# Performance work log

Hardware: AMD Instinct MI355X
Metric: run time of the kernel (lower is better)

Reference implementation:

```python
import jax, jax.numpy as jnp
import numpy as np

NUM_HEADS = 16
WINDOW = 256


def setup_inputs() -> dict:
    key = jax.random.key(0)
    ks = jax.random.split(key, 9)
    B, S, H = 2, 2048, 1024
    sc = 0.02
    return {
        "hidden_states": jax.random.normal(ks[0], (B, S, H), jnp.float32),
        "wq": jax.random.normal(ks[1], (H, H), jnp.float32) * sc,
        "bq": jax.random.normal(ks[2], (H,), jnp.float32) * sc,
        "wk": jax.random.normal(ks[3], (H, H), jnp.float32) * sc,
        "bk": jax.random.normal(ks[4], (H,), jnp.float32) * sc,
        "wv": jax.random.normal(ks[5], (H, H), jnp.float32) * sc,
        "bv": jax.random.normal(ks[6], (H,), jnp.float32) * sc,
        "wo": jax.random.normal(ks[7], (H, H), jnp.float32) * sc,
        "bo": jax.random.normal(ks[8], (H,), jnp.float32) * sc,
    }


def reference(hidden_states, wq, bq, wk, bk, wv, bv, wo, bo):
    B, S, H = hidden_states.shape
    nH, hd = NUM_HEADS, H // NUM_HEADS
    scale = 1.0 / np.sqrt(hd).astype(np.float32)

    def heads(x):  # [B,S,H] -> [B,nH,S,hd]
        return x.reshape(B, S, nH, hd).transpose(0, 2, 1, 3)

    q = heads(hidden_states @ wq.T + bq)
    k = heads(hidden_states @ wk.T + bk)
    v = heads(hidden_states @ wv.T + bv)

    scores = jnp.einsum("bhqd,bhkd->bhqk", q, k) * scale  # [B,nH,S,S]

    # allowed keys for query i: j in [i - WINDOW, i] (causal window)
    i = jnp.arange(S)[:, None]
    j = jnp.arange(S)[None, :]
    allowed = (j <= i) & (j >= i - WINDOW)  # [S,S]

    scores = jnp.where(allowed[None, None], scores, -jnp.inf)
    # original clamps AFTER masking -> -inf becomes -10000 (soft mask)
    scores = jnp.clip(scores, -10000.0, 10000.0)

    probs = jax.nn.softmax(scores, axis=-1)
    probs = jnp.nan_to_num(probs, nan=0.0, posinf=0.0, neginf=0.0)

    out = jnp.einsum("bhqk,bhkd->bhqd", probs, v)  # [B,nH,S,hd]
    out = out.transpose(0, 2, 1, 3).reshape(B, S, H)
    return out @ wo.T + bo
```

## Files before the change

kernel.cpp:

```cpp
#include <hip/hip_runtime.h>
#include <hip/hip_bf16.h>
#include <stdint.h>

typedef __attribute__((ext_vector_type(8))) short short8;
typedef __attribute__((ext_vector_type(4))) float f32x4;
typedef __attribute__((ext_vector_type(4))) unsigned short u16x4;

__device__ __forceinline__ float bf2f(unsigned short u) {
  union { unsigned int u; float f; } x; x.u = ((unsigned int)u) << 16; return x.f;
}
__device__ __forceinline__ unsigned short f2bf(float f) {
  union { float f; unsigned int u; } x; x.f = f;
  unsigned int u = x.u;
  return (unsigned short)((u + 0x7fffu + ((u >> 16) & 1u)) >> 16);
}

__device__ __forceinline__ void gload_lds16(const void* g, void* l) {
  __builtin_amdgcn_global_load_lds(
      (const __attribute__((address_space(1))) void*)g,
      (__attribute__((address_space(3))) void*)l, 16, 0, 0);
}

__global__ void cvt_all(const float* __restrict__ X,
                        const float* __restrict__ w0, const float* __restrict__ w1,
                        const float* __restrict__ w2, const float* __restrict__ w3,
                        unsigned short* __restrict__ Xb,
                        unsigned short* __restrict__ Wb) {
  if (blockIdx.y == 0) {
    int i = (blockIdx.x * 256 + threadIdx.x) * 4;
    f32x4 f = *(const f32x4*)(X + i);
    u16x4 o = { f2bf(f[0]), f2bf(f[1]), f2bf(f[2]), f2bf(f[3]) };
    *(u16x4*)(Xb + i) = o;
  } else {
    int wi = blockIdx.x >> 10;
    const float* s = wi == 0 ? w0 : wi == 1 ? w1 : wi == 2 ? w2 : w3;
    int j = ((blockIdx.x & 1023) * 256 + threadIdx.x) * 4;
    f32x4 f = *(const f32x4*)(s + j);
    u16x4 o = { f2bf(f[0]), f2bf(f[1]), f2bf(f[2]), f2bf(f[3]) };
    *(u16x4*)(Wb + ((size_t)wi << 20) + j) = o;
  }
}

template <int MODE, bool SWAP, int BN>
__device__ __forceinline__ void gemm_body(
    const unsigned short* __restrict__ A, const unsigned short* __restrict__ W,
    const float* __restrict__ bias, unsigned short* __restrict__ obf,
    float* __restrict__ of32, unsigned short* lds, int z) {
  const int K = 1024, NT = 32;
  constexpr int GX = 1024 / BN;
  constexpr int LB = BN / 64;
  constexpr int NWC = BN / 64;
  constexpr int NWR = 4 / NWC;
  constexpr int MS = 128 / NWR;
  constexpr int MR = MS / 16;
  constexpr int ASZ = 128 * 32, BSZ = BN * 32;

  constexpr int NWG = GX * 32;
  int flat = blockIdx.y * GX + blockIdx.x;
  int swz = (flat & 7) * (NWG / 8) + (flat >> 3);
  const int n0 = (swz % GX) * BN, m0 = (swz / GX) * 128;

  const int tid = threadIdx.x, lane = tid & 63, w = tid >> 6;
  const int wr = w / NWC, wc = w % NWC;
  const int fr = lane & 15, g = lane >> 4;

  f32x4 acc[MR][4] = {};

#define STAGE(bi, t)                                                            \
  do {                                                                          \
    unsigned short* lb = lds + (bi) * (ASZ + BSZ);                              \
    _Pragma("unroll") for (int i = 0; i < 2; ++i) {                             \
      int s = i * 256 + tid;                                                    \
      int row = s >> 2;                                                         \
      int gc = (s & 3) ^ ((row >> 1) & 3);                                      \
      gload_lds16(A + (size_t)(m0 + row) * K + (t) * 32 + gc * 8, &lb[s * 8]);  \
    }                                                                           \
    _Pragma("unroll") for (int i = 0; i < LB; ++i) {                            \
      int s = i * 256 + tid;                                                    \
      int row = s >> 2;                                                         \
      int gc = (s & 3) ^ ((row >> 1) & 3);                                      \
      gload_lds16(W + (size_t)(n0 + row) * K + (t) * 32 + gc * 8,               \
                  &lb[ASZ + s * 8]);                                            \
    }                                                                           \
  } while (0)

#define COMPUTE(bi)                                                             \
  do {                                                                          \
    unsigned short* lb = lds + (bi) * (ASZ + BSZ);                              \
    short8 af[MR], bfr[4];                                                      \
    _Pragma("unroll") for (int m = 0; m < MR; ++m) {                            \
      int ra = wr * MS + m * 16 + fr;                                           \
      af[m] = *(const short8*)&lb[ra * 32 + ((g ^ ((ra >> 1) & 3)) * 8)];       \
    }                                                                           \
    _Pragma("unroll") for (int n = 0; n < 4; ++n) {                             \
      int rb2 = wc * 64 + n * 16 + fr;                                          \
      bfr[n] = *(const short8*)&lb[ASZ + rb2 * 32 + ((g ^ ((rb2 >> 1) & 3)) * 8)]; \
    }                                                                           \
    _Pragma("unroll") for (int m = 0; m < MR; ++m)                              \
        _Pragma("unroll") for (int n = 0; n < 4; ++n) {                         \
      if constexpr (SWAP)                                                       \
        acc[m][n] = __builtin_amdgcn_mfma_f32_16x16x32_bf16(bfr[n], af[m],      \
                                                            acc[m][n], 0, 0, 0);\
      else                                                                      \
        acc[m][n] = __builtin_amdgcn_mfma_f32_16x16x32_bf16(af[m], bfr[n],      \
                                                            acc[m][n], 0, 0, 0);\
    }                                                                           \
  } while (0)

  STAGE(0, 0);
  STAGE(1, 1);
  for (int t = 0; t < NT; ++t) {
    if (t < NT - 1) {
      if constexpr (BN == 128)
        asm volatile("s_waitcnt vmcnt(4)" ::: "memory");
      else
        asm volatile("s_waitcnt vmcnt(3)" ::: "memory");
    } else {
      asm volatile("s_waitcnt vmcnt(0)" ::: "memory");
    }
    __builtin_amdgcn_s_barrier();
    __builtin_amdgcn_sched_barrier(0);
    if (t + 2 < NT) STAGE((t + 2) % 3, t + 2);
    __builtin_amdgcn_s_setprio(1);
    COMPUTE(t % 3);
    __builtin_amdgcn_s_setprio(0);
  }
#undef STAGE
#undef COMPUTE

  if constexpr (SWAP) {
#pragma unroll
    for (int m = 0; m < MR; ++m) {
#pragma unroll
      for (int n = 0; n < 4; ++n) {
        int token = m0 + wr * MS + m * 16 + fr;
        int col0 = n0 + wc * 64 + n * 16 + g * 4;
        f32x4 bv = *(const f32x4*)&bias[col0];
        if (MODE == 0) {
          u16x4 pk;
#pragma unroll
          for (int i = 0; i < 4; ++i) pk[i] = f2bf(acc[m][n][i] + bv[i]);
          int hh = col0 >> 6, d0 = col0 & 63;
          int bb = token >> 11, s0 = token & 2047;
          *(u16x4*)&obf[(((size_t)(z * 32 + bb * 16 + hh)) * 2048 + s0) * 64 + d0] = pk;
        } else {
          f32x4 o;
#pragma unroll
          for (int i = 0; i < 4; ++i) o[i] = acc[m][n][i] + bv[i];
          *(f32x4*)&of32[(size_t)token * 1024 + col0] = o;
        }
      }
    }
  } else {
#pragma unroll
    for (int m = 0; m < MR; ++m) {
#pragma unroll
      for (int n = 0; n < 4; ++n) {
        int col = n0 + wc * 64 + n * 16 + fr;
        float bias_v = bias[col];
        int row0 = m0 + wr * MS + m * 16 + g * 4;
        int hh = col >> 6, d = col & 63;
        int bb = row0 >> 11, s0 = row0 & 2047;
        u16x4 pk;
#pragma unroll
        for (int i = 0; i < 4; ++i) pk[i] = f2bf(acc[m][n][i] + bias_v);
        *(u16x4*)&obf[(((size_t)(64 + bb * 16 + hh)) * 64 + d) * 2048 + s0] = pk;
      }
    }
  }
}

__global__ __launch_bounds__(256)
void gemm_qkv(const unsigned short* __restrict__ A,
              const unsigned short* __restrict__ Wbase,
              const float* __restrict__ bq, const float* __restrict__ bk,
              const float* __restrict__ bv, unsigned short* __restrict__ obf) {
  __shared__ unsigned short lds[3 * 8192];
  const int z = blockIdx.z;
  const unsigned short* W = Wbase + ((size_t)z << 20);
  const float* bias = z == 0 ? bq : z == 1 ? bk : bv;
  if (z == 2)
    gemm_body<0, false, 128>(A, W, bias, obf, nullptr, lds, z);
  else
    gemm_body<0, true, 128>(A, W, bias, obf, nullptr, lds, z);
}

__global__ __launch_bounds__(256)
void gemm_oproj(const unsigned short* __restrict__ A,
                const unsigned short* __restrict__ W,
                const float* __restrict__ bo, float* __restrict__ out) {
  __shared__ unsigned short lds[3 * 6144];
  gemm_body<1, true, 64>(A, W, bo, nullptr, out, lds, 0);
}

__global__ __launch_bounds__(256)
void attn_mfma(const unsigned short* __restrict__ QKV, unsigned short* __restrict__ AO) {
  const int S = 2048;
  const int b = blockIdx.z, h = blockIdx.y;
  const int q0 = blockIdx.x * 128;
  const size_t hb = (size_t)(b * 16 + h);
  const unsigned short* Qh = QKV + hb * (S * 64);
  const unsigned short* Kh = QKV + 4194304 + hb * (S * 64);
  const unsigned short* Vt = QKV + 8388608 + hb * (S * 64);

  const int tid = threadIdx.x;
  const int lane = tid & 63, w = tid >> 6;
  const int c = lane & 15, g = lane >> 4;
  const int qw0 = q0 + 32 * w;

  __shared__ unsigned short Plds[4][1024];
  char* Pb = (char*)&Plds[w][0];

  short8 qa[2][2];
#pragma unroll
  for (int mi = 0; mi < 2; ++mi)
#pragma unroll
    for (int cs = 0; cs < 2; ++cs)
      qa[mi][cs] = *(const short8*)(Qh + (size_t)(qw0 + 16 * mi + c) * 64 + 32 * cs + g * 8);

  f32x4 o[2][4] = {};
  float mrow[2][4], lsum[2][4];
#pragma unroll
  for (int mi = 0; mi < 2; ++mi)
#pragma unroll
    for (int r = 0; r < 4; ++r) { mrow[mi][r] = -1e30f; lsum[mi][r] = 0.f; }

  int kt0 = qw0 - 256; if (kt0 < 0) kt0 = 0;
  const int ktlast = qw0;

  short8 kf[2][2], vf[4];
#pragma unroll
  for (int ni = 0; ni < 2; ++ni)
#pragma unroll
    for (int cs = 0; cs < 2; ++cs)
      kf[ni][cs] = *(const short8*)(Kh + (size_t)(kt0 + 16 * ni + c) * 64 + 32 * cs + g * 8);
#pragma unroll
  for (int ni = 0; ni < 4; ++ni)
    vf[ni] = *(const short8*)(Vt + (size_t)(16 * ni + c) * 2048 + kt0 + g * 8);

  for (int kt = kt0; kt <= ktlast; kt += 32) {
    const int ktn = (kt + 32 <= ktlast) ? kt + 32 : kt;
    short8 kfn[2][2], vfn[4];
#pragma unroll
    for (int ni = 0; ni < 2; ++ni)
#pragma unroll
      for (int cs = 0; cs < 2; ++cs)
        kfn[ni][cs] = *(const short8*)(Kh + (size_t)(ktn + 16 * ni + c) * 64 + 32 * cs + g * 8);
#pragma unroll
    for (int ni = 0; ni < 4; ++ni)
      vfn[ni] = *(const short8*)(Vt + (size_t)(16 * ni + c) * 2048 + ktn + g * 8);

    f32x4 sA[2][2] = {};
#pragma unroll
    for (int mi = 0; mi < 2; ++mi)
#pragma unroll
      for (int ni = 0; ni < 2; ++ni)
#pragma unroll
        for (int cs = 0; cs < 2; ++cs)
          sA[mi][ni] = __builtin_amdgcn_mfma_f32_16x16x32_bf16(qa[mi][cs], kf[ni][cs],
                                                               sA[mi][ni], 0, 0, 0);

    float sv[2][2][4];
#pragma unroll
    for (int mi = 0; mi < 2; ++mi)
#pragma unroll
      for (int ni = 0; ni < 2; ++ni)
#pragma unroll
        for (int r = 0; r < 4; ++r) {
          int q = qw0 + 16 * mi + 4 * g + r;
          int k = kt + 16 * ni + c;
          sv[mi][ni][r] = ((unsigned)(q - k) <= 256u) ? sA[mi][ni][r] * 0.125f : -3.0e38f;
        }

#pragma unroll
    for (int mi = 0; mi < 2; ++mi) {
#pragma unroll
      for (int r = 0; r < 4; ++r) {
        float tm = fmaxf(sv[mi][0][r], sv[mi][1][r]);
        tm = fmaxf(tm, __shfl_xor(tm, 1));
        tm = fmaxf(tm, __shfl_xor(tm, 2));
        tm = fmaxf(tm, __shfl_xor(tm, 4));
        tm = fmaxf(tm, __shfl_xor(tm, 8));
        float mnew = fmaxf(mrow[mi][r], tm);
        float sc = __expf(mrow[mi][r] - mnew);
        mrow[mi][r] = mnew;
        float p0 = __expf(sv[mi][0][r] - mnew);
        float p1 = __expf(sv[mi][1][r] - mnew);
        float ps = p0 + p1;
        ps += __shfl_xor(ps, 1);
        ps += __shfl_xor(ps, 2);
        ps += __shfl_xor(ps, 4);
        ps += __shfl_xor(ps, 8);
        lsum[mi][r] = lsum[mi][r] * sc + ps;
#pragma unroll
        for (int ni = 0; ni < 4; ++ni)
          o[mi][ni][r] *= sc;
        int qloc = 16 * mi + 4 * g + r;
        int xr = (qloc & 12) << 2;
        *(unsigned short*)(Pb + ((qloc * 64 + c * 2) ^ xr)) = f2bf(p0);
        *(unsigned short*)(Pb + ((qloc * 64 + 32 + c * 2) ^ xr)) = f2bf(p1);
      }
    }

#pragma unroll
    for (int mi = 0; mi < 2; ++mi) {
      int qloc = 16 * mi + c;
      short8 pa = *(const short8*)(Pb + ((qloc * 64 + g * 16) ^ ((qloc & 12) << 2)));
#pragma unroll
      for (int ni = 0; ni < 4; ++ni)
        o[mi][ni] = __builtin_amdgcn_mfma_f32_16x16x32_bf16(pa, vf[ni], o[mi][ni], 0, 0, 0);
    }

#pragma unroll
    for (int ni = 0; ni < 2; ++ni)
#pragma unroll
      for (int cs = 0; cs < 2; ++cs)
        kf[ni][cs] = kfn[ni][cs];
#pragma unroll
    for (int ni = 0; ni < 4; ++ni)
      vf[ni] = vfn[ni];
  }

#pragma unroll
  for (int mi = 0; mi < 2; ++mi)
#pragma unroll
    for (int r = 0; r < 4; ++r) {
      float inv = 1.f / lsum[mi][r];
      int q = qw0 + 16 * mi + 4 * g + r;
      unsigned short* row = AO + (size_t)(b * 2048 + q) * 1024 + h * 64 + c;
#pragma unroll
      for (int ni = 0; ni < 4; ++ni)
        row[16 * ni] = f2bf(o[mi][ni][r] * inv);
    }
}

extern "C" void kernel_launch(void* const* d_in, const int* in_sizes, int n_in,
                              void* d_out, int out_size, void* d_ws, size_t ws_size,
                              hipStream_t stream) {
  const float* X  = (const float*)d_in[0];
  const float* wq = (const float*)d_in[1];
  const float* bq = (const float*)d_in[2];
  const float* wk = (const float*)d_in[3];
  const float* bk = (const float*)d_in[4];
  const float* wv = (const float*)d_in[5];
  const float* bv = (const float*)d_in[6];
  const float* wo = (const float*)d_in[7];
  const float* bo = (const float*)d_in[8];
  float* out = (float*)d_out;

  unsigned short* Xb  = (unsigned short*)d_ws;
  unsigned short* Wb  = Xb + 4194304;
  unsigned short* QKV = Wb + 4194304;
  unsigned short* AO  = QKV + 12582912;

  cvt_all<<<dim3(4096, 2), dim3(256), 0, stream>>>(X, wq, wk, wv, wo, Xb, Wb);
  gemm_qkv<<<dim3(8, 32, 3), dim3(256), 0, stream>>>(Xb, Wb, bq, bk, bv, QKV);
  attn_mfma<<<dim3(16, 16, 2), dim3(256), 0, stream>>>(QKV, AO);
  gemm_oproj<<<dim3(16, 32, 1), dim3(256), 0, stream>>>(AO, Wb + 3 * 1048576, bo, out);
}
```

Measured before the change: 92.44 us.

## Fuse Q/K/V projections into one GEMM sharing the A tile

```diff
diff --git a/kernel.cpp b/kernel.cpp
--- a/kernel.cpp
+++ b/kernel.cpp
@@ -41,19 +41,135 @@
   }
 }
 
-template <int MODE, bool SWAP, int BN>
-__device__ __forceinline__ void gemm_body(
-    const unsigned short* __restrict__ A, const unsigned short* __restrict__ W,
-    const float* __restrict__ bias, unsigned short* __restrict__ obf,
-    float* __restrict__ of32, unsigned short* lds, int z) {
+__global__ __launch_bounds__(512, 2)
+void gemm_qkv_fused(const unsigned short* __restrict__ A,
+                    const unsigned short* __restrict__ Wbase,
+                    const float* __restrict__ bq, const float* __restrict__ bk,
+                    const float* __restrict__ bv,
+                    unsigned short* __restrict__ obf) {
   const int K = 1024, NT = 32;
+  constexpr int ASZ = 128 * 32;
+  constexpr int BSZ = 3 * 128 * 32;
+  __shared__ unsigned short lds[3 * (ASZ + BSZ)];
+
+  int flat = blockIdx.y * 8 + blockIdx.x;
+  int swz = (flat & 7) * 32 + (flat >> 3);
+  const int n0 = (swz & 7) * 128, m0 = (swz >> 3) * 128;
+
+  const int tid = threadIdx.x, lane = tid & 63, w = tid >> 6;
+  const int wr = w >> 1, wc = w & 1;
+  const int fr = lane & 15, g = lane >> 4;
+
+  f32x4 acc[3][2][4] = {};
+
+#define STAGE(bi, t)                                                            \
+  do {                                                                          \
+    unsigned short* lb = lds + (bi) * (ASZ + BSZ);                              \
+    {                                                                           \
+      int s = tid;                                                              \
+      int row = s >> 2;                                                         \
+      int gc = (s & 3) ^ ((row >> 1) & 3);                                      \
+      gload_lds16(A + (size_t)(m0 + row) * K + (t) * 32 + gc * 8, &lb[s * 8]);  \
+    }                                                                           \
+    _Pragma("unroll") for (int i = 0; i < 3; ++i) {                             \
+      int s = i * 512 + tid;                                                    \
+      int row = s >> 2;                        \
+      int zz = row >> 7, br = row & 127;                                        \
+      int gc = (s & 3) ^ ((row >> 1) & 3);                                      \
+      gload_lds16(Wbase + ((size_t)zz << 20) + (size_t)(n0 + br) * K +          \
+                      (t) * 32 + gc * 8,                                        \
+                  &lb[ASZ + s * 8]);                                            \
+    }                                                                           \
+  } while (0)
+
+#define COMPUTE(bi)                                                             \
+  do {                                                                          \
+    unsigned short* lb = lds + (bi) * (ASZ + BSZ);                              \
+    short8 af[2], bfr[3][4];                                                    \
+    _Pragma("unroll") for (int m = 0; m < 2; ++m) {                             \
+      int ra = wr * 32 + m * 16 + fr;                                           \
+      af[m] = *(const short8*)&lb[ra * 32 + ((g ^ ((ra >> 1) & 3)) * 8)];       \
+    }                                                                           \
+    _Pragma("unroll") for (int zz = 0; zz < 3; ++zz)                            \
+        _Pragma("unroll") for (int n = 0; n < 4; ++n) {                         \
+      int rb2 = zz * 128 + wc * 64 + n * 16 + fr;                               \
+      bfr[zz][n] =                                                              \
+          *(const short8*)&lb[ASZ + rb2 * 32 + ((g ^ ((rb2 >> 1) & 3)) * 8)];   \
+    }                                                                           \
+    _Pragma("unroll") for (int zz = 0; zz < 3; ++zz)                            \
+        _Pragma("unroll") for (int m = 0; m < 2; ++m)                           \
+        _Pragma("unroll") for (int n = 0; n < 4; ++n) {                         \
+      if (zz < 2)                                                               \
+        acc[zz][m][n] = __builtin_amdgcn_mfma_f32_16x16x32_bf16(                \
+            bfr[zz][n], af[m], acc[zz][m][n], 0, 0, 0);                         \
+      else                                                                      \
+        acc[zz][m][n] = __builtin_amdgcn_mfma_f32_16x16x32_bf16(                \
+            af[m], bfr[zz][n], acc[zz][m][n], 0, 0, 0);                         \
+    }                                                                           \
+  } while (0)
+
+  STAGE(0, 0);
+  STAGE(1, 1);
+  for (int t = 0; t < NT; ++t) {
+    if (t < NT - 1)
+      asm volatile("s_waitcnt vmcnt(4)" ::: "memory");
+    else
+      asm volatile("s_waitcnt vmcnt(0)" ::: "memory");
+    __builtin_amdgcn_s_barrier();
+    __builtin_amdgcn_sched_barrier(0);
+    if (t + 2 < NT) STAGE((t + 2) % 3, t + 2);
+    __builtin_amdgcn_s_setprio(1);
+    COMPUTE(t % 3);
+    __builtin_amdgcn_s_setprio(0);
+  }
+#undef STAGE
+#undef COMPUTE
+
+#pragma unroll
+  for (int zz = 0; zz < 2; ++zz) {
+    const float* bias = zz == 0 ? bq : bk;
+#pragma unroll
+    for (int m = 0; m < 2; ++m) {
+#pragma unroll
+      for (int n = 0; n < 4; ++n) {
+        int token = m0 + wr * 32 + m * 16 + fr;
+        int col0 = n0 + wc * 64 + n * 16 + g * 4;
+        f32x4 bvv = *(const f32x4*)&bias[col0];
+        u16x4 pk;
+#pragma unroll
+        for (int i = 0; i < 4; ++i) pk[i] = f2bf(acc[zz][m][n][i] + bvv[i]);
+        int hh = col0 >> 6, d0 = col0 & 63;
+        int bb = token >> 11, s0 = token & 2047;
+        *(u16x4*)&obf[(((size_t)(zz * 32 + bb * 16 + hh)) * 2048 + s0) * 64 + d0] = pk;
+      }
+    }
+  }
+#pragma unroll
+  for (int m = 0; m < 2; ++m) {
+#pragma unroll
+    for (int n = 0; n < 4; ++n) {
+      int col = n0 + wc * 64 + n * 16 + fr;
+      float bias_v = bv[col];
+      int row0 = m0 + wr * 32 + m * 16 + g * 4;
+      int hh = col >> 6, d = col & 63;
+      int bb = row0 >> 11, s0 = row0 & 2047;
+      u16x4 pk;
+#pragma unroll
+      for (int i = 0; i < 4; ++i) pk[i] = f2bf(acc[2][m][n][i] + bias_v);
+      *(u16x4*)&obf[(((size_t)(64 + bb * 16 + hh)) * 64 + d) * 2048 + s0] = pk;
+    }
+  }
+}
+
+__global__ __launch_bounds__(256)
+void gemm_oproj(const unsigned short* __restrict__ A,
+                const unsigned short* __restrict__ W,
+                const float* __restrict__ bias, float* __restrict__ of32) {
+  const int K = 1024, NT = 32;
+  constexpr int BN = 64;
   constexpr int GX = 1024 / BN;
-  constexpr int LB = BN / 64;
-  constexpr int NWC = BN / 64;
-  constexpr int NWR = 4 / NWC;
-  constexpr int MS = 128 / NWR;
-  constexpr int MR = MS / 16;
   constexpr int ASZ = 128 * 32, BSZ = BN * 32;
+  __shared__ unsigned short lds[3 * (ASZ + BSZ)];
 
   constexpr int NWG = GX * 32;
   int flat = blockIdx.y * GX + blockIdx.x;
@@ -61,10 +177,9 @@
   const int n0 = (swz % GX) * BN, m0 = (swz / GX) * 128;
 
   const int tid = threadIdx.x, lane = tid & 63, w = tid >> 6;
-  const int wr = w / NWC, wc = w % NWC;
   const int fr = lane & 15, g = lane >> 4;
 
-  f32x4 acc[MR][4] = {};
+  f32x4 acc[2][4] = {};
 
 #define STAGE(bi, t)                                                            \
   do {                                                                          \
@@ -75,8 +190,8 @@
       int gc = (s & 3) ^ ((row >> 1) & 3);                                      \
       gload_lds16(A + (size_t)(m0 + row) * K + (t) * 32 + gc * 8, &lb[s * 8]);  \
     }                                                                           \
-    _Pragma("unroll") for (int i = 0; i < LB; ++i) {                            \
-      int s = i * 256 + tid;                                                    \
+    {                                                                           \
+      int s = tid;                                                              \
       int row = s >> 2;                                                         \
       int gc = (s & 3) ^ ((row >> 1) & 3);                                      \
       gload_lds16(W + (size_t)(n0 + row) * K + (t) * 32 + gc * 8,               \
@@ -87,37 +202,28 @@
 #define COMPUTE(bi)                                                             \
   do {                                                                          \
     unsigned short* lb = lds + (bi) * (ASZ + BSZ);                              \
-    short8 af[MR], bfr[4];                                                      \
-    _Pragma("unroll") for (int m = 0; m < MR; ++m) {                            \
-      int ra = wr * MS + m * 16 + fr;                                           \
+    short8 af[2], bfr[4];                                                       \
+    _Pragma("unroll") for (int m = 0; m < 2; ++m) {                             \
+      int ra = w * 32 + m * 16 + fr;                                            \
       af[m] = *(const short8*)&lb[ra * 32 + ((g ^ ((ra >> 1) & 3)) * 8)];       \
     }                                                                           \
     _Pragma("unroll") for (int n = 0; n < 4; ++n) {                             \
-      int rb2 = wc * 64 + n * 16 + fr;                                          \
+      int rb2 = n * 16 + fr;                                                    \
       bfr[n] = *(const short8*)&lb[ASZ + rb2 * 32 + ((g ^ ((rb2 >> 1) & 3)) * 8)]; \
     }                                                                           \
-    _Pragma("unroll") for (int m = 0; m < MR; ++m)                              \
-        _Pragma("unroll") for (int n = 0; n < 4; ++n) {                         \
-      if constexpr (SWAP)                                                       \
+    _Pragma("unroll") for (int m = 0; m < 2; ++m)                               \
+        _Pragma("unroll") for (int n = 0; n < 4; ++n)                           \
         acc[m][n] = __builtin_amdgcn_mfma_f32_16x16x32_bf16(bfr[n], af[m],      \
                                                             acc[m][n], 0, 0, 0);\
-      else                                                                      \
-        acc[m][n] = __builtin_amdgcn_mfma_f32_16x16x32_bf16(af[m], bfr[n],      \
-                                                            acc[m][n], 0, 0, 0);\
-    }                                                                           \
   } while (0)
 
   STAGE(0, 0);
   STAGE(1, 1);
   for (int t = 0; t < NT; ++t) {
-    if (t < NT - 1) {
-      if constexpr (BN == 128)
-        asm volatile("s_waitcnt vmcnt(4)" ::: "memory");
-      else
-        asm volatile("s_waitcnt vmcnt(3)" ::: "memory");
-    } else {
+    if (t < NT - 1)
+      asm volatile("s_waitcnt vmcnt(3)" ::: "memory");
+    else
       asm volatile("s_waitcnt vmcnt(0)" ::: "memory");
-    }
     __builtin_amdgcn_s_barrier();
     __builtin_amdgcn_sched_barrier(0);
     if (t + 2 < NT) STAGE((t + 2) % 3, t + 2);
@@ -128,69 +234,19 @@
 #undef STAGE
 #undef COMPUTE
 
-  if constexpr (SWAP) {
-#pragma unroll
-    for (int m = 0; m < MR; ++m) {
-#pragma unroll
-      for (int n = 0; n < 4; ++n) {
-        int token = m0 + wr * MS + m * 16 + fr;
-        int col0 = n0 + wc * 64 + n * 16 + g * 4;
-        f32x4 bv = *(const f32x4*)&bias[col0];
-        if (MODE == 0) {
-          u16x4 pk;
-#pragma unroll
-          for (int i = 0; i < 4; ++i) pk[i] = f2bf(acc[m][n][i] + bv[i]);
-          int hh = col0 >> 6, d0 = col0 & 63;
-          int bb = token >> 11, s0 = token & 2047;
-          *(u16x4*)&obf[(((size_t)(z * 32 + bb * 16 + hh)) * 2048 + s0) * 64 + d0] = pk;
-        } else {
-          f32x4 o;
-#pragma unroll
-          for (int i = 0; i < 4; ++i) o[i] = acc[m][n][i] + bv[i];
-          *(f32x4*)&of32[(size_t)token * 1024 + col0] = o;
-        }
-      }
-    }
-  } else {
-#pragma unroll
-    for (int m = 0; m < MR; ++m) {
-#pragma unroll
-      for (int n = 0; n < 4; ++n) {
-        int col = n0 + wc * 64 + n * 16 + fr;
-        float bias_v = bias[col];
-        int row0 = m0 + wr * MS + m * 16 + g * 4;
-        int hh = col >> 6, d = col & 63;
-        int bb = row0 >> 11, s0 = row0 & 2047;
-        u16x4 pk;
-#pragma unroll
-        for (int i = 0; i < 4; ++i) pk[i] = f2bf(acc[m][n][i] + bias_v);
-        *(u16x4*)&obf[(((size_t)(64 + bb * 16 + hh)) * 64 + d) * 2048 + s0] = pk;
-      }
-    }
-  }
-}
-
-__global__ __launch_bounds__(256)
-void gemm_qkv(const unsigned short* __restrict__ A,
-              const unsigned short* __restrict__ Wbase,
-              const float* __restrict__ bq, const float* __restrict__ bk,
-              const float* __restrict__ bv, unsigned short* __restrict__ obf) {
-  __shared__ unsigned short lds[3 * 8192];
-  const int z = blockIdx.z;
-  const unsigned short* W = Wbase + ((size_t)z << 20);
-  const float* bias = z == 0 ? bq : z == 1 ? bk : bv;
-  if (z == 2)
-    gemm_body<0, false, 128>(A, W, bias, obf, nullptr, lds, z);
-  else
-    gemm_body<0, true, 128>(A, W, bias, obf, nullptr, lds, z);
-}
-
-__global__ __launch_bounds__(256)
-void gemm_oproj(const unsigned short* __restrict__ A,
-                const unsigned short* __restrict__ W,
-                const float* __restrict__ bo, float* __restrict__ out) {
-  __shared__ unsigned short lds[3 * 6144];
-  gemm_body<1, true, 64>(A, W, bo, nullptr, out, lds, 0);
+#pragma unroll
+  for (int m = 0; m < 2; ++m) {
+#pragma unroll
+    for (int n = 0; n < 4; ++n) {
+      int token = m0 + w * 32 + m * 16 + fr;
+      int col0 = n0 + n * 16 + g * 4;
+      f32x4 bvv = *(const f32x4*)&bias[col0];
+      f32x4 o;
+#pragma unroll
+      for (int i = 0; i < 4; ++i) o[i] = acc[m][n][i] + bvv[i];
+      *(f32x4*)&of32[(size_t)token * 1024 + col0] = o;
+    }
+  }
 }
 
 __global__ __launch_bounds__(256)
@@ -354,7 +410,7 @@
   unsigned short* AO  = QKV + 12582912;
 
   cvt_all<<<dim3(4096, 2), dim3(256), 0, stream>>>(X, wq, wk, wv, wo, Xb, Wb);
-  gemm_qkv<<<dim3(8, 32, 3), dim3(256), 0, stream>>>(Xb, Wb, bq, bk, bv, QKV);
+  gemm_qkv_fused<<<dim3(8, 32), dim3(512), 0, stream>>>(Xb, Wb, bq, bk, bv, QKV);
   attn_mfma<<<dim3(16, 16, 2), dim3(256), 0, stream>>>(QKV, AO);
   gemm_oproj<<<dim3(16, 32, 1), dim3(256), 0, stream>>>(AO, Wb + 3 * 1048576, bo, out);
 }
```

New measurement: 89.57 us. 3.1% less time.
